# Optimization experiments

Hardware: AMD Instinct MI355X
Metric: run time of the kernel (lower is better)

## Reference

```python
import jax, jax.numpy as jnp
import numpy as np

DIM = 2048
NUM_EXPERTS = 64
TOP_K = 2


def setup_inputs() -> dict:
    key = jax.random.key(0)
    kx, kw = jax.random.split(key)
    x = jax.random.normal(kx, (4, 8192, DIM), dtype=jnp.float32)
    # nn.Linear(dim, num_experts, bias=False) -> weight [num_experts, dim]
    W = jax.random.normal(kw, (NUM_EXPERTS, DIM), dtype=jnp.float32) * (1.0 / np.sqrt(DIM))
    return {"x": x, "W": W}


def reference(x, W):
    # gate scores: [B, S, E]
    gate_scores = jnp.einsum("bsd,ed->bse", x, W)
    # top-k over experts
    top_k_values, top_k_indices = jax.lax.top_k(gate_scores, TOP_K)
    top_k_weights = jax.nn.softmax(top_k_values, axis=-1)  # [B, S, K]
    # load-balancing aux loss
    expert_usage = jax.nn.softmax(gate_scores, axis=-1).mean(axis=(0, 1))  # [E]
    aux_loss = NUM_EXPERTS * jnp.sum(expert_usage ** 2)
    return (top_k_indices, top_k_weights, aux_loss)
```

## Files before the change

kernel.cpp:

```cpp
#include <hip/hip_runtime.h>

#define DIM    2048
#define NE     64
#define NTOK   32768
#define BM     64
#define NTHR   256
#define KW     512
#define NKC    16
#define S      68
#define WPLANE (NE*DIM)

typedef __attribute__((ext_vector_type(8))) short short8;
typedef __attribute__((ext_vector_type(4))) float f32x4;

union U4S8 { uint4 u; short8 s; };

__device__ __forceinline__ unsigned pack_hi16(unsigned e0, unsigned e1) {
    return __builtin_amdgcn_perm(e1, e0, 0x07060302u);
}

__device__ __forceinline__ void split8(const float4& a, const float4& b,
                                       short8& h, short8& m, short8& l) {
    const float f[8] = {a.x, a.y, a.z, a.w, b.x, b.y, b.z, b.w};
    unsigned hb[8], mb[8], lb[8];
#pragma unroll
    for (int j = 0; j < 8; ++j) {
        const unsigned xb = __float_as_uint(f[j]);
        const unsigned th = xb & 0xffff0000u;
        const float    rh = f[j] - __uint_as_float(th);
        const unsigned rb = __float_as_uint(rh);
        const unsigned tm = rb & 0xffff0000u;
        const float    rm = rh - __uint_as_float(tm);
        hb[j] = th; mb[j] = tm; lb[j] = __float_as_uint(rm);
    }
    U4S8 H, M, L;
    H.u = make_uint4(pack_hi16(hb[0],hb[1]), pack_hi16(hb[2],hb[3]),
                     pack_hi16(hb[4],hb[5]), pack_hi16(hb[6],hb[7]));
    M.u = make_uint4(pack_hi16(mb[0],mb[1]), pack_hi16(mb[2],mb[3]),
                     pack_hi16(mb[4],mb[5]), pack_hi16(mb[6],mb[7]));
    L.u = make_uint4(pack_hi16(lb[0],lb[1]), pack_hi16(lb[2],lb[3]),
                     pack_hi16(lb[4],lb[5]), pack_hi16(lb[6],lb[7]));
    h = H.s; m = M.s; l = L.s;
}

__global__ void router_wsplit(const float* __restrict__ W, unsigned short* __restrict__ W3)
{
    const int i = blockIdx.x * 256 + threadIdx.x;
    const float f = W[i];
    const unsigned xb = __float_as_uint(f);
    const unsigned th = xb & 0xffff0000u;
    const float    rh = f - __uint_as_float(th);
    const unsigned rb = __float_as_uint(rh);
    const unsigned tm = rb & 0xffff0000u;
    const float    rm = rh - __uint_as_float(tm);
    W3[i]            = (unsigned short)(th >> 16);
    W3[WPLANE + i]   = (unsigned short)(tm >> 16);
    W3[2*WPLANE + i] = (unsigned short)(__float_as_uint(rm) >> 16);
}

struct SmemEpi { float ps[4][BM * S]; float mx[BM]; float zinv[BM]; float us[4][NE]; };

#define MFMA_GROUP(AF, BF)                                                       \
    _Pragma("unroll") for (int nt = 0; nt < 4; ++nt)                             \
    _Pragma("unroll") for (int mt = 0; mt < 4; ++mt)                             \
        acc[mt][nt] = __builtin_amdgcn_mfma_f32_16x16x32_bf16(                   \
            AF[mt], BF[nt].s, acc[mt][nt], 0, 0, 0);

__global__ __launch_bounds__(NTHR, 2)
void router_main(const float* __restrict__ x, const unsigned short* __restrict__ W3,
                 float* __restrict__ out_idx, float* __restrict__ out_w,
                 float* __restrict__ gusage)
{
    __shared__ SmemEpi sm;
    const int tid  = threadIdx.x;
    const int w    = tid >> 6;
    const int ln   = tid & 63;
    const int q    = ln >> 4;
    const int c    = ln & 15;
    const int tok0 = blockIdx.x * BM;
    const int kbase = w * KW + q * 8;

    const float* xr[4];
#pragma unroll
    for (int mt = 0; mt < 4; ++mt)
        xr[mt] = x + (size_t)(tok0 + mt*16 + c) * DIM + kbase;
    const unsigned short* wr[4];
#pragma unroll
    for (int nt = 0; nt < 4; ++nt)
        wr[nt] = W3 + (size_t)(nt*16 + c) * DIM + kbase;

    f32x4 acc[4][4];
#pragma unroll
    for (int mt = 0; mt < 4; ++mt)
#pragma unroll
        for (int nt = 0; nt < 4; ++nt)
            acc[mt][nt] = (f32x4){0.f, 0.f, 0.f, 0.f};

    float4 xf0[4], xf1[4];
#pragma unroll
    for (int mt = 0; mt < 4; ++mt) {
        xf0[mt] = *(const float4*)(xr[mt]);
        xf1[mt] = *(const float4*)(xr[mt] + 4);
    }

    for (int kc = 0; kc < NKC; ++kc) {
        const int ko = kc * 32;
        U4S8 bh[4];
#pragma unroll
        for (int nt = 0; nt < 4; ++nt) bh[nt].u = *(const uint4*)(wr[nt] + ko);

        short8 ah[4], am[4], al[4];
#pragma unroll
        for (int mt = 0; mt < 4; ++mt) split8(xf0[mt], xf1[mt], ah[mt], am[mt], al[mt]);

        if (kc + 1 < NKC) {
#pragma unroll
            for (int mt = 0; mt < 4; ++mt) {
                xf0[mt] = *(const float4*)(xr[mt] + ko + 32);
                xf1[mt] = *(const float4*)(xr[mt] + ko + 36);
            }
        }

        U4S8 bm[4];
#pragma unroll
        for (int nt = 0; nt < 4; ++nt) bm[nt].u = *(const uint4*)(wr[nt] + WPLANE + ko);

        MFMA_GROUP(ah, bh)
        MFMA_GROUP(am, bh)
        MFMA_GROUP(al, bh)

        U4S8 bl[4];
#pragma unroll
        for (int nt = 0; nt < 4; ++nt) bl[nt].u = *(const uint4*)(wr[nt] + 2*WPLANE + ko);

        MFMA_GROUP(ah, bm)
        MFMA_GROUP(am, bm)
        MFMA_GROUP(ah, bl)
    }

    {
        float* ps = sm.ps[w];
#pragma unroll
        for (int mt = 0; mt < 4; ++mt)
#pragma unroll
            for (int r = 0; r < 4; ++r) {
                const int t = mt*16 + q*4 + r;
#pragma unroll
                for (int nt = 0; nt < 4; ++nt)
                    ps[t*S + nt*16 + c] = acc[mt][nt][r];
            }
    }
    __syncthreads();
    {
        const int t = tid & 63;
        const int qq = tid >> 6;
        float* p0 = sm.ps[0];
#pragma unroll
        for (int e0 = 0; e0 < 16; ++e0) {
            const int idx = t*S + (qq*16 + e0);
            p0[idx] += sm.ps[1][idx] + sm.ps[2][idx] + sm.ps[3][idx];
        }
    }
    __syncthreads();

    const float* sc = sm.ps[0];
    if (tid < BM) {
        const int t = tid;
        float v1 = -3.4e38f, v2 = -3.4e38f;
        int   i1 = 0, i2 = 0;
        for (int e = 0; e < NE; ++e) {
            float s = sc[t*S + e];
            if (s > v1)      { v2 = v1; i2 = i1; v1 = s; i1 = e; }
            else if (s > v2) { v2 = s;  i2 = e; }
        }
        float z = 0.f;
        for (int e = 0; e < NE; ++e) z += __expf(sc[t*S + e] - v1);
        sm.mx[t]   = v1;
        sm.zinv[t] = 1.f / z;

        const int gt = tok0 + t;
        out_idx[gt*2 + 0] = (float)i1;
        out_idx[gt*2 + 1] = (float)i2;
        float e21 = __expf(v2 - v1);
        float w1  = 1.f / (1.f + e21);
        out_w[gt*2 + 0] = w1;
        out_w[gt*2 + 1] = e21 * w1;
    }
    __syncthreads();

    {
        const int e  = tid & 63;
        const int cc = tid >> 6;
        float u = 0.f;
        const int tbeg = cc * 16;
        for (int t = tbeg; t < tbeg + 16; ++t)
            u += __expf(sc[t*S + e] - sm.mx[t]) * sm.zinv[t];
        sm.us[cc][e] = u;
    }
    __syncthreads();
    if (tid < NE) {
        float u = sm.us[0][tid] + sm.us[1][tid] + sm.us[2][tid] + sm.us[3][tid];
        atomicAdd(&gusage[tid], u);
    }
}

__global__ void router_finalize(const float* __restrict__ gusage, float* __restrict__ out_aux)
{
    const int e = threadIdx.x;
    float u = gusage[e] * (1.0f / (float)NTOK);
    float s = u * u;
#pragma unroll
    for (int off = 32; off > 0; off >>= 1)
        s += __shfl_down(s, off, 64);
    if (e == 0) out_aux[0] = (float)NE * s;
}

extern "C" void kernel_launch(void* const* d_in, const int* in_sizes, int n_in,
                              void* d_out, int out_size, void* d_ws, size_t ws_size,
                              hipStream_t stream)
{
    const float* x = (const float*)d_in[0];
    const float* W = (const float*)d_in[1];
    float* out     = (float*)d_out;
    float* out_idx = out;
    float* out_w   = out + NTOK * 2;
    float* out_aux = out + NTOK * 4;

    unsigned short* W3 = (unsigned short*)d_ws;
    float* gusage = (float*)((char*)d_ws + 3 * WPLANE * sizeof(unsigned short));

    hipMemsetAsync(gusage, 0, NE * sizeof(float), stream);
    hipLaunchKernelGGL(router_wsplit, dim3(WPLANE / 256), dim3(256), 0, stream, W, W3);
    hipLaunchKernelGGL(router_main, dim3(NTOK / BM), dim3(NTHR), 0, stream,
                       x, W3, out_idx, out_w, gusage);
    hipLaunchKernelGGL(router_finalize, dim3(1), dim3(NE), 0, stream, gusage, out_aux);
}
```

Measured before the change: 392.4 us.

## Stage split weights in LDS via direct global-to-LDS loads with 32x32 MFMA

The main kernel now stages the three bf16 weight planes in a double-buffered LDS tile, filled with global_load_lds, instead of each wave reading weights straight from global memory. It moves from 16x16x32 to 32x32x16 MFMA tiles, uses 512 threads split across token halves and K quarters, and raises the occupancy target. The aim is to cut redundant global weight traffic and register pressure so more waves can hide the latency of streaming x. In exchange it adds a barrier every K step and a serialized four-pass reduction of the partial scores through LDS.

```diff
diff --git a/kernel.cpp b/kernel.cpp
--- a/kernel.cpp
+++ b/kernel.cpp
@@ -1,23 +1,35 @@
 #include <hip/hip_runtime.h>
+#include <stdint.h>
 
 #define DIM    2048
 #define NE     64
 #define NTOK   32768
 #define BM     64
-#define NTHR   256
-#define KW     512
-#define NKC    16
+#define NTHR   512
+#define KQ     512
+#define BK     16
+#define NIT    (KQ/BK)
+#define WPLANE (NE*DIM)
 #define S      68
-#define WPLANE (NE*DIM)
-
-typedef __attribute__((ext_vector_type(8))) short short8;
-typedef __attribute__((ext_vector_type(4))) float f32x4;
-
-union U4S8 { uint4 u; short8 s; };
+#define WSBUF  24576
+
+typedef __attribute__((ext_vector_type(8)))  short  short8;
+typedef __attribute__((ext_vector_type(16))) float  f32x16;
+
+typedef __attribute__((address_space(3))) void lds_void_t;
+typedef __attribute__((address_space(1))) void gbl_void_t;
+
+__device__ __forceinline__ void gload_lds16(const void* gptr, void* lptr) {
+    __builtin_amdgcn_global_load_lds((gbl_void_t*)(uintptr_t)gptr,
+                                     (lds_void_t*)(uint32_t)(uintptr_t)lptr,
+                                     16, 0, 0);
+}
 
 __device__ __forceinline__ unsigned pack_hi16(unsigned e0, unsigned e1) {
     return __builtin_amdgcn_perm(e1, e0, 0x07060302u);
 }
+
+union U4S8 { uint4 u; short8 s; };
 
 __device__ __forceinline__ void split8(const float4& a, const float4& b,
                                        short8& h, short8& m, short8& l) {
@@ -58,125 +70,124 @@
     W3[2*WPLANE + i] = (unsigned short)(__float_as_uint(rm) >> 16);
 }
 
-struct SmemEpi { float ps[4][BM * S]; float mx[BM]; float zinv[BM]; float us[4][NE]; };
-
-#define MFMA_GROUP(AF, BF)                                                       \
-    _Pragma("unroll") for (int nt = 0; nt < 4; ++nt)                             \
-    _Pragma("unroll") for (int mt = 0; mt < 4; ++mt)                             \
-        acc[mt][nt] = __builtin_amdgcn_mfma_f32_16x16x32_bf16(                   \
-            AF[mt], BF[nt].s, acc[mt][nt], 0, 0, 0);
-
-__global__ __launch_bounds__(NTHR, 2)
+#define MFMA(A, B, C) __builtin_amdgcn_mfma_f32_32x32x16_bf16(A, B, C, 0, 0, 0)
+
+__global__ __launch_bounds__(NTHR, 4)
 void router_main(const float* __restrict__ x, const unsigned short* __restrict__ W3,
                  float* __restrict__ out_idx, float* __restrict__ out_w,
                  float* __restrict__ gusage)
 {
-    __shared__ SmemEpi sm;
+    __shared__ __align__(16) unsigned char smem[2 * WSBUF];
+
     const int tid  = threadIdx.x;
     const int w    = tid >> 6;
     const int ln   = tid & 63;
-    const int q    = ln >> 4;
-    const int c    = ln & 15;
+    const int wk   = w & 3;
+    const int wi   = w >> 2;
     const int tok0 = blockIdx.x * BM;
-    const int kbase = w * KW + q * 8;
-
-    const float* xr[4];
-#pragma unroll
-    for (int mt = 0; mt < 4; ++mt)
-        xr[mt] = x + (size_t)(tok0 + mt*16 + c) * DIM + kbase;
-    const unsigned short* wr[4];
-#pragma unroll
-    for (int nt = 0; nt < 4; ++nt)
-        wr[nt] = W3 + (size_t)(nt*16 + c) * DIM + kbase;
-
-    f32x4 acc[4][4];
-#pragma unroll
-    for (int mt = 0; mt < 4; ++mt)
-#pragma unroll
-        for (int nt = 0; nt < 4; ++nt)
-            acc[mt][nt] = (f32x4){0.f, 0.f, 0.f, 0.f};
-
-    float4 xf0[4], xf1[4];
-#pragma unroll
-    for (int mt = 0; mt < 4; ++mt) {
-        xf0[mt] = *(const float4*)(xr[mt]);
-        xf1[mt] = *(const float4*)(xr[mt] + 4);
-    }
-
-    for (int kc = 0; kc < NKC; ++kc) {
-        const int ko = kc * 32;
-        U4S8 bh[4];
-#pragma unroll
-        for (int nt = 0; nt < 4; ++nt) bh[nt].u = *(const uint4*)(wr[nt] + ko);
-
-        short8 ah[4], am[4], al[4];
-#pragma unroll
-        for (int mt = 0; mt < 4; ++mt) split8(xf0[mt], xf1[mt], ah[mt], am[mt], al[mt]);
-
-        if (kc + 1 < NKC) {
-#pragma unroll
-            for (int mt = 0; mt < 4; ++mt) {
-                xf0[mt] = *(const float4*)(xr[mt] + ko + 32);
-                xf1[mt] = *(const float4*)(xr[mt] + ko + 36);
-            }
-        }
-
-        U4S8 bm[4];
-#pragma unroll
-        for (int nt = 0; nt < 4; ++nt) bm[nt].u = *(const uint4*)(wr[nt] + WPLANE + ko);
-
-        MFMA_GROUP(ah, bh)
-        MFMA_GROUP(am, bh)
-        MFMA_GROUP(al, bh)
-
-        U4S8 bl[4];
-#pragma unroll
-        for (int nt = 0; nt < 4; ++nt) bl[nt].u = *(const uint4*)(wr[nt] + 2*WPLANE + ko);
-
-        MFMA_GROUP(ah, bm)
-        MFMA_GROUP(am, bm)
-        MFMA_GROUP(ah, bl)
-    }
-
-    {
-        float* ps = sm.ps[w];
-#pragma unroll
-        for (int mt = 0; mt < 4; ++mt)
-#pragma unroll
-            for (int r = 0; r < 4; ++r) {
-                const int t = mt*16 + q*4 + r;
-#pragma unroll
-                for (int nt = 0; nt < 4; ++nt)
-                    ps[t*S + nt*16 + c] = acc[mt][nt][r];
-            }
-    }
+    const int arow  = ln & 31;
+    const int ahalf = ln >> 5;
+
+    const int ep = ln >> 1, sb = ln & 1;
+    uint32_t     ws_lb[3];
+    const unsigned short* ws_g[3];
+#pragma unroll
+    for (int i = 0; i < 3; ++i) {
+        const int j = w*3 + i, q = j/6, rem = j%6, p = rem>>1, eh = rem&1;
+        const int e = eh*32 + ep;
+        ws_lb[i] = (uint32_t)((q*3 + p) * 2048 + eh*1024);
+        ws_g[i]  = W3 + (size_t)p*WPLANE + (size_t)e*DIM + q*KQ + ((sb ^ (ep & 1)) * 8);
+    }
+
+    const float* xp = x + (size_t)(tok0 + wi*32 + arow) * DIM + wk*KQ + ahalf*8;
+
+    const int bphys = ahalf ^ (arow & 1);
+    uint32_t b_off[2][3];
+#pragma unroll
+    for (int nt = 0; nt < 2; ++nt)
+#pragma unroll
+        for (int p = 0; p < 3; ++p)
+            b_off[nt][p] = (uint32_t)((wk*3 + p)*2048 + (nt*32 + arow)*32 + bphys*16);
+
+    f32x16 acc[2];
+#pragma unroll
+    for (int nt = 0; nt < 2; ++nt)
+#pragma unroll
+        for (int r = 0; r < 16; ++r) acc[nt][r] = 0.f;
+
+    float4 xa = *(const float4*)(xp);
+    float4 xb = *(const float4*)(xp + 4);
+
+#pragma unroll
+    for (int i = 0; i < 3; ++i)
+        gload_lds16(ws_g[i], smem + ws_lb[i]);
     __syncthreads();
-    {
-        const int t = tid & 63;
-        const int qq = tid >> 6;
-        float* p0 = sm.ps[0];
-#pragma unroll
-        for (int e0 = 0; e0 < 16; ++e0) {
-            const int idx = t*S + (qq*16 + e0);
-            p0[idx] += sm.ps[1][idx] + sm.ps[2][idx] + sm.ps[3][idx];
-        }
-    }
-    __syncthreads();
-
-    const float* sc = sm.ps[0];
+
+    for (int kt = 0; kt < NIT; ++kt) {
+        const int buf = kt & 1;
+        if (kt + 1 < NIT) {
+            const unsigned char* dst = smem + (1 - buf) * WSBUF;
+#pragma unroll
+            for (int i = 0; i < 3; ++i)
+                gload_lds16(ws_g[i] + (kt + 1) * BK, (void*)(dst + ws_lb[i]));
+        }
+
+        short8 ah, am, al;
+        split8(xa, xb, ah, am, al);
+        if (kt + 1 < NIT) {
+            xa = *(const float4*)(xp + (kt + 1) * BK);
+            xb = *(const float4*)(xp + (kt + 1) * BK + 4);
+        }
+
+        const unsigned char* wb = smem + buf * WSBUF;
+#pragma unroll
+        for (int nt = 0; nt < 2; ++nt) {
+            const short8 bh = *(const short8*)(wb + b_off[nt][0]);
+            const short8 bm = *(const short8*)(wb + b_off[nt][1]);
+            const short8 bl = *(const short8*)(wb + b_off[nt][2]);
+            acc[nt] = MFMA(ah, bh, acc[nt]);
+            acc[nt] = MFMA(am, bh, acc[nt]);
+            acc[nt] = MFMA(al, bh, acc[nt]);
+            acc[nt] = MFMA(ah, bm, acc[nt]);
+            acc[nt] = MFMA(am, bm, acc[nt]);
+            acc[nt] = MFMA(ah, bl, acc[nt]);
+        }
+        __syncthreads();
+    }
+
+    float* ps  = (float*)smem;
+    float* mxa = (float*)(smem + 17408);
+    float* zia = (float*)(smem + 17664);
+    float* usa = (float*)(smem + 17920);
+
+    for (int pass = 0; pass < 4; ++pass) {
+        if (wk == pass) {
+#pragma unroll
+            for (int nt = 0; nt < 2; ++nt)
+#pragma unroll
+                for (int r = 0; r < 16; ++r) {
+                    const int t = wi*32 + (r & 3) + 8*(r >> 2) + 4*ahalf;
+                    const int e = nt*32 + arow;
+                    if (pass == 0) ps[t*S + e]  = acc[nt][r];
+                    else           ps[t*S + e] += acc[nt][r];
+                }
+        }
+        __syncthreads();
+    }
+
     if (tid < BM) {
         const int t = tid;
         float v1 = -3.4e38f, v2 = -3.4e38f;
         int   i1 = 0, i2 = 0;
         for (int e = 0; e < NE; ++e) {
-            float s = sc[t*S + e];
+            float s = ps[t*S + e];
             if (s > v1)      { v2 = v1; i2 = i1; v1 = s; i1 = e; }
             else if (s > v2) { v2 = s;  i2 = e; }
         }
         float z = 0.f;
-        for (int e = 0; e < NE; ++e) z += __expf(sc[t*S + e] - v1);
-        sm.mx[t]   = v1;
-        sm.zinv[t] = 1.f / z;
+        for (int e = 0; e < NE; ++e) z += __expf(ps[t*S + e] - v1);
+        mxa[t] = v1;
+        zia[t] = 1.f / z;
 
         const int gt = tok0 + t;
         out_idx[gt*2 + 0] = (float)i1;
@@ -189,17 +200,18 @@
     __syncthreads();
 
     {
-        const int e  = tid & 63;
-        const int cc = tid >> 6;
+        const int e = tid & 63;
+        const int c = tid >> 6;
         float u = 0.f;
-        const int tbeg = cc * 16;
-        for (int t = tbeg; t < tbeg + 16; ++t)
-            u += __expf(sc[t*S + e] - sm.mx[t]) * sm.zinv[t];
-        sm.us[cc][e] = u;
+        for (int t = c*8; t < c*8 + 8; ++t)
+            u += __expf(ps[t*S + e] - mxa[t]) * zia[t];
+        usa[c*64 + e] = u;
     }
     __syncthreads();
     if (tid < NE) {
-        float u = sm.us[0][tid] + sm.us[1][tid] + sm.us[2][tid] + sm.us[3][tid];
+        float u = 0.f;
+#pragma unroll
+        for (int c = 0; c < 8; ++c) u += usa[c*64 + tid];
         atomicAdd(&gusage[tid], u);
     }
 }
```

Measured after the change: 396.3 us. No clear change (+1.0%).
